# Kernel tuning notes

Measured on AMD Instinct MI355X. Metric: run time of the kernel, lower is better.

The kernel has to match this reference:

```python
import jax, jax.numpy as jnp
from jax import lax
import numpy as np

VOCAB = 100000
MAX_SEQ = 8192
DIM = 128
K = 5
STRIDE = 1
PAD = 2


def setup_inputs() -> dict:
    key = jax.random.key(0)
    ks = jax.random.split(key, 6)
    X = jax.random.randint(ks[0], (8, 8192), 0, VOCAB, dtype=jnp.int64)
    # nn.Linear(vocab, dim): weight (dim, vocab), bias (dim)
    W_lin = jax.random.normal(ks[1], (DIM, VOCAB), dtype=jnp.float32) * 0.02
    b_lin = jax.random.normal(ks[2], (DIM,), dtype=jnp.float32) * 0.02
    # nn.Conv1d(dim, dim, k): weight (out=dim, in=dim, k), bias (dim)
    W_conv = jax.random.normal(ks[3], (DIM, DIM, K), dtype=jnp.float32) * 0.02
    b_conv = jax.random.normal(ks[4], (DIM,), dtype=jnp.float32) * 0.02
    # nn.Embedding(max_seq_len, dim)
    pos_table = jax.random.normal(ks[5], (MAX_SEQ, DIM), dtype=jnp.float32) * 0.02
    return {"X": X, "W_lin": W_lin, "b_lin": b_lin,
            "W_conv": W_conv, "b_conv": b_conv, "pos_table": pos_table}


def reference(X, W_lin, b_lin, W_conv, b_conv, pos_table):
    # one_hot(X) @ W_lin.T + b_lin  ==  gather rows of W_lin.T
    emb = jnp.take(W_lin.T, X, axis=0) + b_lin          # (b, n, d)
    x = jnp.transpose(emb, (0, 2, 1))                   # (b, d, n)
    y = lax.conv_general_dilated(
        x, W_conv, window_strides=(STRIDE,), padding=[(PAD, PAD)],
        dimension_numbers=("NCH", "OIH", "NCH"))
    y = y + b_conv[None, :, None]                       # (b, d, n_out)
    tokens = jnp.transpose(y, (0, 2, 1))                # (b, n_out, d)
    n_out = tokens.shape[1]
    return tokens + pos_table[:n_out][None, :, :]
```

## Files before the change

kernel.cpp:

```cpp
#include <hip/hip_runtime.h>
#include <hip/hip_bf16.h>
#include <stdint.h>

#define VOCAB 100000
#define SEQ   8192
#define BATCH 8
#define DIM   128
#define NB_WLT 1563

typedef short bf16x8 __attribute__((ext_vector_type(8)));
typedef float f32x4  __attribute__((ext_vector_type(4)));

__device__ __forceinline__ ushort f2bf(float f) {
  union { float f; uint32_t u; } v; v.f = f;
  uint32_t u = v.u;
  return (ushort)((u + 0x7FFF + ((u >> 16) & 1)) >> 16);
}

__global__ __launch_bounds__(256) void build_tables(
    const float* __restrict__ wlin, const float* __restrict__ blin,
    const float* __restrict__ wconv, ushort* __restrict__ wlt,
    ushort* __restrict__ wcb) {
  __shared__ float tile[128 * 65];
  const int tid = threadIdx.x;

  if (blockIdx.x >= NB_WLT) {
    int e = (blockIdx.x - NB_WLT) * 1024 + tid;
#pragma unroll
    for (int i = 0; i < 4; ++i, e += 256) {
      if (e < 5 * DIM * DIM) {
        int k = e >> 14;
        int rem = e & 16383;
        int d = rem >> 7, ii = rem & 127;
        wcb[e] = f2bf(wconv[(d * DIM + ii) * 5 + k]);
      }
    }
    return;
  }

  const int t0 = blockIdx.x * 64;

  const int c4 = (tid & 15) * 4;
  const int rbase = tid >> 4;
  const bool cvalid = (t0 + c4) < VOCAB;
#pragma unroll
  for (int p = 0; p < 8; ++p) {
    int r = p * 16 + rbase;
    float4 v = make_float4(0.f, 0.f, 0.f, 0.f);
    if (cvalid) v = *(const float4*)(wlin + (size_t)r * VOCAB + t0 + c4);
    float* dst = &tile[r * 65 + c4];
    dst[0] = v.x; dst[1] = v.y; dst[2] = v.z; dst[3] = v.w;
  }
  __syncthreads();

  const int chunk = tid & 15;
  float bias8[8];
#pragma unroll
  for (int j = 0; j < 8; ++j) bias8[j] = blin[chunk * 8 + j];

#pragma unroll
  for (int p = 0; p < 4; ++p) {
    int tl = (tid >> 4) + p * 16;
    int t  = t0 + tl;
    if (t >= VOCAB) continue;
    ushort u[8];
#pragma unroll
    for (int j = 0; j < 8; ++j) {
      float f = tile[(chunk * 8 + j) * 65 + tl] + bias8[j];
      u[j] = f2bf(f);
    }
    *(uint4*)(wlt + (size_t)t * DIM + chunk * 8) = *(const uint4*)u;
  }
}

__global__ __launch_bounds__(256, 4) void conv_main(
    const int* __restrict__ X, const ushort* __restrict__ wlt,
    const ushort* __restrict__ wcb, const float* __restrict__ bconv,
    const float* __restrict__ pos, float* __restrict__ out) {
  __shared__ __align__(16) ushort Atile[68 * 136];

  const int tid   = threadIdx.x;
  const int bm    = blockIdx.x;
  const int batch = bm >> 7;
  const int nbase = (bm & 127) << 6;
  const int* Xb   = X + batch * SEQ;

  int  tok[5];
  bool valid[5];
#pragma unroll
  for (int it = 0; it < 5; ++it) {
    int c = tid + it * 256;
    int r = c >> 4;
    int n = nbase - 2 + r;
    bool v = (c < 1088) && (n >= 0) && (n < SEQ);
    valid[it] = v;
    tok[it] = v ? Xb[n] : 0;
  }
  uint4 val[5];
#pragma unroll
  for (int it = 0; it < 5; ++it) {
    int c = tid + it * 256;
    int ch = c & 15;
    val[it] = valid[it] ? *(const uint4*)(wlt + (size_t)tok[it] * DIM + ch * 8)
                        : make_uint4(0u, 0u, 0u, 0u);
  }
#pragma unroll
  for (int it = 0; it < 5; ++it) {
    int c = tid + it * 256;
    if (c < 1088) {
      int r = c >> 4, ch = c & 15;
      *(uint4*)&Atile[r * 136 + ch * 8] = val[it];
    }
  }
  __syncthreads();

  const int wave = tid >> 6;
  const int lane = tid & 63;
  const int wn = wave << 5;
  const int lr = lane & 15;
  const int lq = lane >> 4;

  f32x4 acc[4][2];
#pragma unroll
  for (int a = 0; a < 4; ++a)
#pragma unroll
    for (int b = 0; b < 2; ++b) acc[a][b] = (f32x4)0.f;

#pragma unroll
  for (int k = 0; k < 5; ++k) {
    bf16x8 B[2][4];
#pragma unroll
    for (int nt = 0; nt < 2; ++nt)
#pragma unroll
      for (int kk = 0; kk < 4; ++kk)
        B[nt][kk] = *(const bf16x8*)(wcb +
            ((size_t)(k * DIM + wn + nt * 16 + lr) * DIM + kk * 32 + lq * 8));
#pragma unroll
    for (int kk = 0; kk < 4; ++kk) {
      bf16x8 A[4];
#pragma unroll
      for (int mt = 0; mt < 4; ++mt)
        A[mt] = *(const bf16x8*)&Atile[(mt * 16 + lr + k) * 136 + kk * 32 + lq * 8];
#pragma unroll
      for (int mt = 0; mt < 4; ++mt)
#pragma unroll
        for (int nt = 0; nt < 2; ++nt)
          acc[mt][nt] = __builtin_amdgcn_mfma_f32_16x16x32_bf16(
              B[nt][kk], A[mt], acc[mt][nt], 0, 0, 0);
    }
  }

  float* outb = out + (size_t)batch * SEQ * DIM;
#pragma unroll
  for (int nt = 0; nt < 2; ++nt) {
    int d0 = wn + nt * 16 + lq * 4;
    const f32x4 bc4 = *(const f32x4*)(bconv + d0);
#pragma unroll
    for (int mt = 0; mt < 4; ++mt) {
      int gn = nbase + mt * 16 + lr;
      const f32x4 p4 = *(const f32x4*)(pos + (size_t)gn * DIM + d0);
      f32x4 v = acc[mt][nt] + bc4 + p4;
      *(f32x4*)(outb + (size_t)gn * DIM + d0) = v;
    }
  }
}

extern "C" void kernel_launch(void* const* d_in, const int* in_sizes, int n_in,
                              void* d_out, int out_size, void* d_ws, size_t ws_size,
                              hipStream_t stream) {
  const int*   X     = (const int*)d_in[0];
  const float* wlin  = (const float*)d_in[1];
  const float* blin  = (const float*)d_in[2];
  const float* wconv = (const float*)d_in[3];
  const float* bconv = (const float*)d_in[4];
  const float* pos   = (const float*)d_in[5];
  float*       out   = (float*)d_out;

  ushort* wcb = (ushort*)d_ws;
  ushort* wlt = (ushort*)((char*)d_ws + 262144);

  hipLaunchKernelGGL(build_tables, dim3(NB_WLT + 80), dim3(256), 0, stream,
                     wlin, blin, wconv, wlt, wcb);
  hipLaunchKernelGGL(conv_main, dim3(1024), dim3(256), 0, stream,
                     X, wlt, wcb, bconv, pos, out);
}
```

Before: 140.2 us.

## Split conv output channels across two blocks for more parallelism and occupancy

```diff
diff --git a/kernel.cpp b/kernel.cpp
--- a/kernel.cpp
+++ b/kernel.cpp
@@ -73,7 +73,7 @@
   }
 }
 
-__global__ __launch_bounds__(256, 4) void conv_main(
+__global__ __launch_bounds__(256, 6) void conv_main(
     const int* __restrict__ X, const ushort* __restrict__ wlt,
     const ushort* __restrict__ wcb, const float* __restrict__ bconv,
     const float* __restrict__ pos, float* __restrict__ out) {
@@ -81,8 +81,10 @@
 
   const int tid   = threadIdx.x;
   const int bm    = blockIdx.x;
-  const int batch = bm >> 7;
-  const int nbase = (bm & 127) << 6;
+  const int batch = bm >> 8;
+  const int rem   = bm & 255;
+  const int nbase = (rem >> 1) << 6;
+  const int dbase = (rem & 1) << 6;
   const int* Xb   = X + batch * SEQ;
 
   int  tok[5];
@@ -116,25 +118,21 @@
 
   const int wave = tid >> 6;
   const int lane = tid & 63;
-  const int wn = wave << 5;
+  const int wn = dbase + (wave << 4);
   const int lr = lane & 15;
   const int lq = lane >> 4;
 
-  f32x4 acc[4][2];
+  f32x4 acc[4];
 #pragma unroll
-  for (int a = 0; a < 4; ++a)
-#pragma unroll
-    for (int b = 0; b < 2; ++b) acc[a][b] = (f32x4)0.f;
+  for (int a = 0; a < 4; ++a) acc[a] = (f32x4)0.f;
 
 #pragma unroll
   for (int k = 0; k < 5; ++k) {
-    bf16x8 B[2][4];
+    bf16x8 B[4];
 #pragma unroll
-    for (int nt = 0; nt < 2; ++nt)
-#pragma unroll
-      for (int kk = 0; kk < 4; ++kk)
-        B[nt][kk] = *(const bf16x8*)(wcb +
-            ((size_t)(k * DIM + wn + nt * 16 + lr) * DIM + kk * 32 + lq * 8));
+    for (int kk = 0; kk < 4; ++kk)
+      B[kk] = *(const bf16x8*)(wcb +
+          ((size_t)(k * DIM + wn + lr) * DIM + kk * 32 + lq * 8));
 #pragma unroll
     for (int kk = 0; kk < 4; ++kk) {
       bf16x8 A[4];
@@ -143,25 +141,20 @@
         A[mt] = *(const bf16x8*)&Atile[(mt * 16 + lr + k) * 136 + kk * 32 + lq * 8];
 #pragma unroll
       for (int mt = 0; mt < 4; ++mt)
-#pragma unroll
-        for (int nt = 0; nt < 2; ++nt)
-          acc[mt][nt] = __builtin_amdgcn_mfma_f32_16x16x32_bf16(
-              B[nt][kk], A[mt], acc[mt][nt], 0, 0, 0);
+        acc[mt] = __builtin_amdgcn_mfma_f32_16x16x32_bf16(
+            B[kk], A[mt], acc[mt], 0, 0, 0);
     }
   }
 
   float* outb = out + (size_t)batch * SEQ * DIM;
+  const int d0 = wn + lq * 4;
+  const f32x4 bc4 = *(const f32x4*)(bconv + d0);
 #pragma unroll
-  for (int nt = 0; nt < 2; ++nt) {
-    int d0 = wn + nt * 16 + lq * 4;
-    const f32x4 bc4 = *(const f32x4*)(bconv + d0);
-#pragma unroll
-    for (int mt = 0; mt < 4; ++mt) {
-      int gn = nbase + mt * 16 + lr;
-      const f32x4 p4 = *(const f32x4*)(pos + (size_t)gn * DIM + d0);
-      f32x4 v = acc[mt][nt] + bc4 + p4;
-      *(f32x4*)(outb + (size_t)gn * DIM + d0) = v;
-    }
+  for (int mt = 0; mt < 4; ++mt) {
+    int gn = nbase + mt * 16 + lr;
+    const f32x4 p4 = *(const f32x4*)(pos + (size_t)gn * DIM + d0);
+    f32x4 v = acc[mt] + bc4 + p4;
+    *(f32x4*)(outb + (size_t)gn * DIM + d0) = v;
   }
 }
 
@@ -181,6 +174,6 @@
 
   hipLaunchKernelGGL(build_tables, dim3(NB_WLT + 80), dim3(256), 0, stream,
                      wlin, blin, wconv, wlt, wcb);
-  hipLaunchKernelGGL(conv_main, dim3(1024), dim3(256), 0, stream,
+  hipLaunchKernelGGL(conv_main, dim3(2048), dim3(256), 0, stream,
                      X, wlt, wcb, bconv, pos, out);
 }
```

Measured after the change: 140.5 us. No clear change (+0.2%).
